# Performance work log

Hardware: AMD Instinct MI355X
Metric: run time of the kernel (lower is better)

## Reference

```python
import jax, jax.numpy as jnp
import numpy as np

EPS = 1e-12  # F.normalize eps


def _l2norm(v, axis=-1):
    # torch.nn.functional.normalize: x / max(||x||_2, eps)
    n = jnp.sqrt(jnp.sum(v * v, axis=axis, keepdims=True))
    return v / jnp.maximum(n, EPS)


def setup_inputs() -> dict:
    key = jax.random.key(0)
    ks = jax.random.split(key, 4)
    B, C, W, H, Z = 8, 256, 16, 16, 16
    N, P = W * H * Z, 64
    heads = 8
    import math
    std_w = 1.0 / math.sqrt(C)      # nn.Linear default-ish scale
    std_ef = 1.0 / math.sqrt(P)     # init_() uses last-dim
    return {
        "x": jax.random.normal(ks[0], (B, C, W, H, Z), dtype=jnp.float32),
        "W_sa": jax.random.uniform(ks[1], (4 * C, C), jnp.float32, -std_w, std_w),
        "EF": jax.random.uniform(ks[2], (N, P), jnp.float32, -std_ef, std_ef),
        "temp2_sa": jnp.ones((heads, 1, 1), jnp.float32),
        "W_sc": jax.random.uniform(ks[3], (4 * C, C), jnp.float32, -std_w, std_w),
        "temp_sc": jnp.ones((heads, 1, 1), jnp.float32),
    }


def _qkvv(xf, Wt, heads):
    # xf: (B, N, C); torch Linear(hidden, 4*hidden, bias=False): y = x @ W.T
    B, N, C = xf.shape
    d = C // heads
    y = xf @ Wt.T                                   # (B, N, 4C)
    y = y.reshape(B, N, 4, heads, d)
    y = jnp.transpose(y, (2, 0, 3, 1, 4))           # (4, B, h, N, d)
    return y[0], y[1], y[2], y[3]


def reference(x, W_sa, EF, temp2_sa, W_sc, temp_sc):
    B, C, W, H, Z = x.shape
    N = W * H * Z
    heads = temp_sc.shape[0]
    d = C // heads
    xf = jnp.transpose(x.reshape(B, C, N), (0, 2, 1))  # (B, N, C)

    # ---- Spatial (Linformer-style projected) attention ----
    q, k, _, v_sa = _qkvv(xf, W_sa, heads)            # each (B, h, N, d)
    q_t = jnp.swapaxes(q, -2, -1)                     # (B, h, d, N)
    k_t = jnp.swapaxes(k, -2, -1)
    v_t = jnp.swapaxes(v_sa, -2, -1)
    k_proj = jnp.einsum('bhdn,nk->bhdk', k_t, EF)     # (B, h, d, P)
    v_proj = jnp.einsum('bhdn,nk->bhdk', v_t, EF)
    q_n = _l2norm(q_t, axis=-1)                       # normalize over N
    attn_sa = jnp.einsum('bhdn,bhdk->bhnk', q_n, k_proj) * temp2_sa  # (B,h,N,P)
    attn_sa = jax.nn.softmax(attn_sa, axis=-1)        # dropout: eval mode (identity)
    x_sa = jnp.einsum('bhnk,bhdk->bhnd', attn_sa, v_proj)            # (B,h,N,d)
    # faithful to original: permute(0,3,1,2) then reshape(B,N,C)
    x_sa = jnp.transpose(x_sa, (0, 3, 1, 2)).reshape(B, N, C)

    # ---- Channel (cross-covariance) attention ----
    qc, kc, v_ca, _ = _qkvv(xf, W_sc, heads)          # (B, h, N, d)
    qc_t = _l2norm(jnp.swapaxes(qc, -2, -1), axis=-1) # (B, h, d, N), norm over N
    kc_t = _l2norm(jnp.swapaxes(kc, -2, -1), axis=-1)
    vc_t = jnp.swapaxes(v_ca, -2, -1)                 # (B, h, d, N)
    attn_ca = jnp.einsum('bhdn,bhen->bhde', qc_t, kc_t) * temp_sc    # (B,h,d,d)
    attn_ca = jax.nn.softmax(attn_ca, axis=-1)
    x_ca = jnp.einsum('bhde,bhen->bhdn', attn_ca, vc_t)              # (B,h,d,N)
    x_ca = jnp.transpose(x_ca, (0, 3, 1, 2)).reshape(B, N, C)        # (B,N,h,d)->(B,N,C)

    feat = x_ca + x_sa
    out = jnp.transpose(feat.reshape(B, W, H, Z, C), (0, 4, 1, 2, 3))
    return out
```

## Files before the change

### kernel.cpp

```cpp
#include <hip/hip_runtime.h>

typedef unsigned short u16;
typedef unsigned int   u32;

typedef __attribute__((ext_vector_type(4))) short short4v;
typedef __attribute__((ext_vector_type(8))) short bf16x8;
typedef __attribute__((ext_vector_type(4))) float f32x4;


__device__ __forceinline__ float bf2f(u16 u){
  union { u32 i; float f; } v; v.i = ((u32)u) << 16; return v.f;
}
__device__ __forceinline__ u16 f2bf(float f){
  u32 u = __float_as_uint(f);
  u32 r = u + 0x7FFFu + ((u >> 16) & 1u);
  return (u16)(r >> 16);
}

__device__ __forceinline__ void gload_lds16(const u16* g, u16* l){
  __builtin_amdgcn_global_load_lds((const __attribute__((address_space(1))) void*)g,
                                   (__attribute__((address_space(3))) void*)l,
                                   16, 0, 0);
}

__global__ void k_detect(const u16* __restrict__ x, u32* __restrict__ flag){
  __shared__ int cnt[256];
  const int t = threadIdx.x;
  int c = 0;
  #pragma unroll
  for(int i = 0; i < 4; i++){
    u16 v = x[t * 4 + i];
    int e = (v >> 7) & 0xFF;
    if(e >= 112 && e <= 134) c++;
  }
  cnt[t] = c;
  __syncthreads();
  for(int s = 128; s > 0; s >>= 1){
    if(t < s) cnt[t] += cnt[t + s];
    __syncthreads();
  }
  if(t == 0) *flag = (cnt[0] < 800) ? 1u : 0u;
}

__global__ __launch_bounds__(256) void k_conv_bf(const void* __restrict__ src,
                                                 u16* __restrict__ dst, int n,
                                                 const u32* __restrict__ flag){
  const int i0 = (blockIdx.x * 256 + threadIdx.x) * 8;
  if(i0 >= n) return;
  const bool isf32 = (*flag != 0);
  if(isf32){
    const float4 a = *(const float4*)((const float*)src + i0);
    const float4 b = *(const float4*)((const float*)src + i0 + 4);
    uint4 o;
    o.x = (u32)f2bf(a.x) | ((u32)f2bf(a.y) << 16);
    o.y = (u32)f2bf(a.z) | ((u32)f2bf(a.w) << 16);
    o.z = (u32)f2bf(b.x) | ((u32)f2bf(b.y) << 16);
    o.w = (u32)f2bf(b.z) | ((u32)f2bf(b.w) << 16);
    *(uint4*)(dst + i0) = o;
  } else {
    *(uint4*)(dst + i0) = *(const uint4*)((const u16*)src + i0);
  }
}

__global__ __launch_bounds__(256) void k_conv_both(const void* __restrict__ src,
                                                   float* __restrict__ dstf,
                                                   u16* __restrict__ dstb, int n,
                                                   int nb,
                                                   const u32* __restrict__ flag){
  const int i0 = (blockIdx.x * 256 + threadIdx.x) * 4;
  if(i0 >= n) return;
  const bool isf32 = (*flag != 0);
  float4 o;
  if(isf32){
    o = *(const float4*)((const float*)src + i0);
  } else {
    const uint2 a = *(const uint2*)((const u16*)src + i0);
    o.x = bf2f((u16)(a.x & 0xFFFF)); o.y = bf2f((u16)(a.x >> 16));
    o.z = bf2f((u16)(a.y & 0xFFFF)); o.w = bf2f((u16)(a.y >> 16));
  }
  *(float4*)(dstf + i0) = o;
  if(i0 < nb){
    uint2 pk;
    pk.x = (u32)f2bf(o.x) | ((u32)f2bf(o.y) << 16);
    pk.y = (u32)f2bf(o.z) | ((u32)f2bf(o.w) << 16);
    *(uint2*)(dstb + i0) = pk;
  }
}

__global__ void k_conv_tf(const void* __restrict__ s0, const void* __restrict__ s1,
                          float* __restrict__ tf, const u32* __restrict__ flag){
  const int t = threadIdx.x;
  if(t >= 16) return;
  const void* s = (t < 8) ? s0 : s1;
  const int i = t & 7;
  if(*flag != 0) tf[t] = ((const float*)s)[i];
  else           tf[t] = bf2f(((const u16*)s)[i]);
}

__global__ __launch_bounds__(256) void k_convT(const void* __restrict__ src,
                                               u16* __restrict__ xb,
                                               u16* __restrict__ xT,
                                               const u32* __restrict__ flag){
  __shared__ u16 T[64][72];
  const int t = threadIdx.x;
  const int n0 = blockIdx.x * 64, c0 = blockIdx.y * 64, b = blockIdx.z;
  const int cl = t >> 2, ns = (t & 3) * 16;
  const bool isf32 = (*flag != 0);
  const size_t srcoff = ((size_t)(b * 256 + c0 + cl)) * 4096 + n0 + ns;
  u16 e[16];
  if(isf32){
    const float* sp = (const float*)src + srcoff;
    #pragma unroll
    for(int i = 0; i < 4; i++){
      const float4 v = *(const float4*)(sp + i * 4);
      e[i*4+0] = f2bf(v.x); e[i*4+1] = f2bf(v.y);
      e[i*4+2] = f2bf(v.z); e[i*4+3] = f2bf(v.w);
    }
  } else {
    const u16* sp = (const u16*)src + srcoff;
    *(uint4*)&e[0] = *(const uint4*)sp;
    *(uint4*)&e[8] = *(const uint4*)(sp + 8);
  }
  u16* xbp = xb + srcoff;
  *(uint4*)xbp       = *(uint4*)&e[0];
  *(uint4*)(xbp + 8) = *(uint4*)&e[8];
  #pragma unroll
  for(int i = 0; i < 16; i++) T[ns + i][cl] = e[i];
  __syncthreads();
  const int nl = t >> 2, cs = (t & 3) * 16;
  u16* xtp = xT + ((size_t)b * 4096 + n0 + nl) * 256 + c0 + cs;
  *(uint4*)xtp       = *(const uint4*)&T[nl][cs];
  *(uint4*)(xtp + 8) = *(const uint4*)&T[nl][cs + 8];
}

__global__ __launch_bounds__(256) void k_conv_efT(const void* __restrict__ src,
                                                  u16* __restrict__ EFT,
                                                  const u32* __restrict__ flag){
  __shared__ u16 T[64][72];
  const int t = threadIdx.x;
  const int n0 = blockIdx.x * 64;
  const int nl = t >> 2, p0 = (t & 3) * 16;
  const bool isf32 = (*flag != 0);
  const size_t off = (size_t)(n0 + nl) * 64 + p0;
  u16 e[16];
  if(isf32){
    const float* sp = (const float*)src + off;
    #pragma unroll
    for(int i = 0; i < 4; i++){
      const float4 v = *(const float4*)(sp + i * 4);
      e[i*4+0] = f2bf(v.x); e[i*4+1] = f2bf(v.y);
      e[i*4+2] = f2bf(v.z); e[i*4+3] = f2bf(v.w);
    }
  } else {
    const u16* sp = (const u16*)src + off;
    *(uint4*)&e[0] = *(const uint4*)sp;
    *(uint4*)&e[8] = *(const uint4*)(sp + 8);
  }
  #pragma unroll
  for(int i = 0; i < 16; i++) T[p0 + i][nl] = e[i];
  __syncthreads();
  const int pr = t >> 2, nn = (t & 3) * 16;
  u16* dp = EFT + (size_t)pr * 4096 + n0 + nn;
  *(uint4*)dp       = *(const uint4*)&T[pr][nn];
  *(uint4*)(dp + 8) = *(const uint4*)&T[pr][nn + 8];
}

__global__ __launch_bounds__(256) void k_qkv(const u16* __restrict__ Wc,
                                             const u16* __restrict__ xT,
                                             u16* __restrict__ Y){
  __shared__ union {
    struct { u16 Ws[128][64]; u16 Xs[128][64]; } s;
    u16 Cs[128][136];
  } L;
  const int t = threadIdx.x;
  const int n0 = blockIdx.x * 128, m0 = blockIdx.y * 128, b = blockIdx.z;
  const int w = t >> 6, lane = t & 63;
  const int fm = lane & 15, fq = lane >> 4;
  const int wm = w >> 1, wn = w & 1;
  const int lr = lane >> 3, lc = (lane & 7) * 8;
  const u16* gw = Wc + (size_t)m0 * 256;
  const u16* gx = xT + ((size_t)b * 4096 + n0) * 256;
  f32x4 acc[4][4] = {};
  for(int kc = 0; kc < 256; kc += 64){
    #pragma unroll
    for(int i = 0; i < 4; i++){
      const int row = w * 32 + i * 8;
      gload_lds16(gw + (size_t)(row + lr) * 256 + kc + lc, &L.s.Ws[row][0]);
      gload_lds16(gx + (size_t)(row + lr) * 256 + kc + lc, &L.s.Xs[row][0]);
    }
    __syncthreads();
    #pragma unroll
    for(int kh = 0; kh < 2; kh++){
      bf16x8 af[4], bx[4];
      #pragma unroll
      for(int mt = 0; mt < 4; mt++)
        af[mt] = *(const bf16x8*)&L.s.Ws[wm * 64 + mt * 16 + fm][kh * 32 + fq * 8];
      #pragma unroll
      for(int nt = 0; nt < 4; nt++)
        bx[nt] = *(const bf16x8*)&L.s.Xs[wn * 64 + nt * 16 + fm][kh * 32 + fq * 8];
      #pragma unroll
      for(int mt = 0; mt < 4; mt++)
        #pragma unroll
        for(int nt = 0; nt < 4; nt++)
          acc[mt][nt] = __builtin_amdgcn_mfma_f32_16x16x32_bf16(af[mt], bx[nt],
                                                                acc[mt][nt], 0, 0, 0);
    }
    __syncthreads();
  }
  #pragma unroll
  for(int mt = 0; mt < 4; mt++)
    #pragma unroll
    for(int nt = 0; nt < 4; nt++)
      #pragma unroll
      for(int r = 0; r < 4; r++)
        L.Cs[wm * 64 + mt * 16 + fq * 4 + r][wn * 64 + nt * 16 + fm] =
          f2bf(acc[mt][nt][r]);
  __syncthreads();
  #pragma unroll
  for(int i = 0; i < 8; i++){
    const int row = i * 16 + (t >> 4), ce = (t & 15) * 8;
    *(uint4*)(Y + ((size_t)b * 1024 + m0 + row) * 4096 + n0 + ce) =
      *(const uint4*)&L.Cs[row][ce];
  }
}

__global__ __launch_bounds__(256) void k_xef_mfma(const u16* __restrict__ xb,
                                                  const u16* __restrict__ EFT,
                                                  float* __restrict__ xefp){
  const int t = threadIdx.x;
  const int mh = blockIdx.x, s = blockIdx.y, b = blockIdx.z;
  const int w = t >> 6, lane = t & 63;
  const int fm = lane & 15, fq = lane >> 4;
  const int c0 = mh * 128 + w * 32;
  const u16* ar = xb + ((size_t)(b * 256 + c0 + fm)) * 4096 + s * 256 + fq * 8;
  const u16* br = EFT + (size_t)fm * 4096 + s * 256 + fq * 8;
  f32x4 acc[2][4] = {};
  #pragma unroll
  for(int kk = 0; kk < 8; kk++){
    bf16x8 bfr[4];
    #pragma unroll
    for(int nt = 0; nt < 4; nt++)
      bfr[nt] = *(const bf16x8*)(br + (size_t)nt * 16 * 4096 + kk * 32);
    #pragma unroll
    for(int mt = 0; mt < 2; mt++){
      bf16x8 af = *(const bf16x8*)(ar + (size_t)mt * 16 * 4096 + kk * 32);
      #pragma unroll
      for(int nt = 0; nt < 4; nt++)
        acc[mt][nt] = __builtin_amdgcn_mfma_f32_16x16x32_bf16(af, bfr[nt],
                                                              acc[mt][nt], 0, 0, 0);
    }
  }
  float* dst = xefp + (size_t)s * 131072 + (size_t)(b * 256 + c0) * 64;
  #pragma unroll
  for(int mt = 0; mt < 2; mt++)
    #pragma unroll
    for(int nt = 0; nt < 4; nt++)
      #pragma unroll
      for(int r = 0; r < 4; r++)
        dst[(mt * 16 + fq * 4 + r) * 64 + nt * 16 + fm] = acc[mt][nt][r];
}

__global__ __launch_bounds__(256) void k_xred(const float* __restrict__ xefp,
                                              float* __restrict__ xef){
  const int i0 = (blockIdx.x * 256 + threadIdx.x) * 4;
  float4 a = *(const float4*)(xefp + i0);
  #pragma unroll
  for(int s = 1; s < 16; s++){
    const float4 v = *(const float4*)(xefp + (size_t)s * 131072 + i0);
    a.x += v.x; a.y += v.y; a.z += v.z; a.w += v.w;
  }
  *(float4*)(xef + i0) = a;
}

__global__ __launch_bounds__(256) void k_kv4b(const float* __restrict__ Wsaf,
                                              const float* __restrict__ xef,
                                              const float* __restrict__ invsa,
                                              u16* __restrict__ kpT,
                                              u16* __restrict__ vpb){
  const int t = threadIdx.x;
  const int ri = t >> 6, p = t & 63;
  const int r = blockIdx.x * 4 + ri, b = blockIdx.y;
  const int row_w = (r < 256) ? (256 + r) : (512 + r);
  const float* wr = Wsaf + (size_t)row_w * 256;
  const float* xr = xef + (size_t)(b * 256) * 64 + p;
  float acc = 0.f;
  for(int c = 0; c < 256; c++)
    acc += wr[c] * xr[(size_t)c * 64];
  if(r < 256){
    const float sc = invsa[b * 256 + r];
    kpT[((size_t)(b * 8 + (r >> 5)) * 64 + p) * 32 + (r & 31)] = f2bf(acc * sc);
  } else {
    const int rv = r - 256;
    vpb[((size_t)(b * 8 + (rv >> 5)) * 32 + (rv & 31)) * 64 + p] = f2bf(acc);
  }
}

__global__ __launch_bounds__(256) void k_norm3(const u16* __restrict__ Y,
                                               float* __restrict__ inv3){
  __shared__ float red[256];
  const int r = blockIdx.x, b = blockIdx.y, t = threadIdx.x;
  const u16* row = Y + (size_t)(b * 1024 + r) * 4096 + t * 16;
  u16 e[16];
  *(uint4*)&e[0] = *(const uint4*)row;
  *(uint4*)&e[8] = *(const uint4*)(row + 8);
  float s = 0.f;
  #pragma unroll
  for(int i = 0; i < 16; i++){ float v = bf2f(e[i]); s += v * v; }
  red[t] = s;
  __syncthreads();
  for(int s2 = 128; s2 > 0; s2 >>= 1){
    if(t < s2) red[t] += red[t + s2];
    __syncthreads();
  }
  if(t == 0)
    inv3[(r >> 8) * 2048 + b * 256 + (r & 255)] =
      1.0f / fmaxf(sqrtf(red[0]), 1e-12f);
}

__device__ __forceinline__ bf16x8 ld_frag8(const u16* p){
  short4v lo = *(const short4v*)p;
  short4v hi = *(const short4v*)(p + 4);
  bf16x8 r;
  r[0]=lo[0]; r[1]=lo[1]; r[2]=lo[2]; r[3]=lo[3];
  r[4]=hi[0]; r[5]=hi[1]; r[6]=hi[2]; r[7]=hi[3];
  return r;
}

__global__ __launch_bounds__(256) void k_gram_mfma(const u16* __restrict__ Y,
                                                   float* __restrict__ Gp){
  const int t = threadIdx.x;
  const int s = blockIdx.x, h = blockIdx.y, b = blockIdx.z;
  const int w = t >> 6, lane = t & 63;
  const int fm = lane & 15, fq = lane >> 4;
  const int j0 = (w >> 1) * 16, e0 = (w & 1) * 16;
  const u16* qrow = Y + (size_t)(b * 1024 + 256 + h * 32 + j0 + fm) * 4096;
  const u16* krow = Y + (size_t)(b * 1024 + 512 + h * 32 + e0 + fm) * 4096;
  f32x4 acc = {};
  const int nb0 = s * 512 + fq * 8;
  #pragma unroll 4
  for(int it = 0; it < 16; it++){
    const int nb = nb0 + it * 32;
    bf16x8 a  = ld_frag8(qrow + nb);
    bf16x8 bb = ld_frag8(krow + nb);
    acc = __builtin_amdgcn_mfma_f32_16x16x32_bf16(a, bb, acc, 0, 0, 0);
  }
  float* dst = Gp + ((size_t)((s * 8 + b) * 8 + h) * 1024);
  #pragma unroll
  for(int r = 0; r < 4; r++)
    dst[(j0 + fq * 4 + r) * 32 + e0 + fm] = acc[r];
}

__global__ void k_softmax_ca(const float* __restrict__ Gp,
                             const float* __restrict__ invq,
                             const float* __restrict__ invk,
                             const float* __restrict__ temp,
                             float* __restrict__ attn){
  const int j = threadIdx.x, h = blockIdx.x, b = blockIdx.y;
  const float tm = temp[h];
  const float iq = invq[b * 256 + h * 32 + j];
  float v[32];
  float m = -1e30f;
  #pragma unroll
  for(int e = 0; e < 32; e++){
    float g = 0.f;
    #pragma unroll
    for(int s = 0; s < 8; s++)
      g += Gp[(size_t)s * 65536 + (size_t)(b * 8 + h) * 1024 + j * 32 + e];
    float val = g * iq * invk[b * 256 + h * 32 + e] * tm;
    v[e] = val; m = fmaxf(m, val);
  }
  float sum = 0.f;
  #pragma unroll
  for(int e = 0; e < 32; e++){ v[e] = __expf(v[e] - m); sum += v[e]; }
  const float inv = 1.0f / sum;
  #pragma unroll
  for(int e = 0; e < 32; e++) attn[(size_t)(b * 8 + h) * 1024 + j * 32 + e] = v[e] * inv;
}

__global__ __launch_bounds__(256) void k_sa_mfma(const u16* __restrict__ Y,
                                                 const u16* __restrict__ kpT,
                                                 const u16* __restrict__ vpb,
                                                 const float* __restrict__ temp2,
                                                 u16* __restrict__ xsa){
  __shared__ u16 As[64][36];
  __shared__ u16 Ks[64][36];
  __shared__ u16 Vs[32][68];
  __shared__ u16 Ps[64][68];
  __shared__ u16 Cs[32][68];
  const int t = threadIdx.x;
  const int ntile = blockIdx.x, h = blockIdx.y, b = blockIdx.z;
  const int n0 = ntile * 64;
  const int w = t >> 6, lane = t & 63;
  const int fm = lane & 15, fq = lane >> 4;
  {
    const int j = t >> 3, ns = (t & 7) * 8;
    const u16* src = Y + (size_t)(b * 1024 + h * 32 + j) * 4096 + n0 + ns;
    uint4 v = *(const uint4*)src;
    u16 e[8]; *(uint4*)e = v;
    #pragma unroll
    for(int i = 0; i < 8; i++) As[ns + i][j] = e[i];
  }
  {
    const int p = t >> 2, jb = (t & 3) * 8;
    *(uint4*)&Ks[p][jb] =
      *(const uint4*)(kpT + ((size_t)(b * 8 + h) * 64 + p) * 32 + jb);
  }
  {
    const int jv = t >> 3, ps = (t & 7) * 8;
    *(uint4*)&Vs[jv][ps] =
      *(const uint4*)(vpb + ((size_t)(b * 8 + h) * 32 + jv) * 64 + ps);
  }
  __syncthreads();
  bf16x8 a = ld_frag8(&As[w * 16 + fm][fq * 8]);
  f32x4 lg[4];
  #pragma unroll
  for(int pt = 0; pt < 4; pt++){
    bf16x8 bk = ld_frag8(&Ks[pt * 16 + fm][fq * 8]);
    f32x4 z = {};
    lg[pt] = __builtin_amdgcn_mfma_f32_16x16x32_bf16(a, bk, z, 0, 0, 0);
  }
  const float tm = temp2[h];
  float sinv[4];
  #pragma unroll
  for(int r = 0; r < 4; r++){
    float v0 = lg[0][r]*tm, v1 = lg[1][r]*tm, v2 = lg[2][r]*tm, v3 = lg[3][r]*tm;
    float mx = fmaxf(fmaxf(v0, v1), fmaxf(v2, v3));
    #pragma unroll
    for(int m = 1; m < 16; m <<= 1) mx = fmaxf(mx, __shfl_xor(mx, m, 16));
    v0 = __expf(v0 - mx); v1 = __expf(v1 - mx);
    v2 = __expf(v2 - mx); v3 = __expf(v3 - mx);
    float s = v0 + v1 + v2 + v3;
    #pragma unroll
    for(int m = 1; m < 16; m <<= 1) s += __shfl_xor(s, m, 16);
    sinv[r] = 1.0f / s;
    const int nrow = w * 16 + fq * 4 + r;
    Ps[nrow][fm]      = f2bf(v0);
    Ps[nrow][16 + fm] = f2bf(v1);
    Ps[nrow][32 + fm] = f2bf(v2);
    Ps[nrow][48 + fm] = f2bf(v3);
  }
  f32x4 o[2] = {};
  #pragma unroll
  for(int ks = 0; ks < 2; ks++){
    bf16x8 ap = ld_frag8(&Ps[w * 16 + fm][ks * 32 + fq * 8]);
    #pragma unroll
    for(int jt = 0; jt < 2; jt++){
      bf16x8 bv = ld_frag8(&Vs[jt * 16 + fm][ks * 32 + fq * 8]);
      o[jt] = __builtin_amdgcn_mfma_f32_16x16x32_bf16(ap, bv, o[jt], 0, 0, 0);
    }
  }
  #pragma unroll
  for(int jt = 0; jt < 2; jt++)
    #pragma unroll
    for(int r = 0; r < 4; r++)
      Cs[jt * 16 + fm][w * 16 + fq * 4 + r] = f2bf(o[jt][r] * sinv[r]);
  __syncthreads();
  {
    const int jv = t >> 3, ns = (t & 7) * 8;
    u16 e[8];
    #pragma unroll
    for(int i = 0; i < 8; i++) e[i] = Cs[jv][ns + i];
    *(uint4*)(xsa + ((size_t)(b * 8 + h) * 32 + jv) * 4096 + n0 + ns) = *(uint4*)e;
  }
}

__global__ __launch_bounds__(256) void k_out_mfma(const u16* __restrict__ Y,
                                                  const float* __restrict__ attn,
                                                  const u16* __restrict__ xsa,
                                                  float* __restrict__ out){
  __shared__ u16 Vt[32][516];
  __shared__ u16 xs[32][16][34];
  __shared__ u16 Ah[32][40];
  __shared__ u16 Al[32][40];
  const int t = threadIdx.x;
  const int jg = blockIdx.x, hc = blockIdx.y, b = blockIdx.z;
  const int nn0 = jg * 512;
  const int w = t >> 6, lane = t & 63;
  const int fm = lane & 15, fq = lane >> 4;
  {
    const float4 v = *(const float4*)(attn + (size_t)(b * 8 + hc) * 1024 + t * 4);
    const int j = t >> 3, e0 = (t & 7) * 4;
    float vv[4] = {v.x, v.y, v.z, v.w};
    #pragma unroll
    for(int i = 0; i < 4; i++){
      u16 hi = f2bf(vv[i]);
      Ah[j][e0 + i] = hi;
      Al[j][e0 + i] = f2bf(vv[i] - bf2f(hi));
    }
  }
  {
    const int e = t >> 3, ch = (t & 7) * 64;
    const u16* src = Y + (size_t)(b * 1024 + 768 + hc * 32 + e) * 4096 + nn0 + ch;
    #pragma unroll
    for(int i = 0; i < 8; i++){
      uint4 v = *(const uint4*)(src + i * 8);
      uint2 lo; lo.x = v.x; lo.y = v.y;
      uint2 hi; hi.x = v.z; hi.y = v.w;
      *(uint2*)&Vt[e][ch + i * 8]     = lo;
      *(uint2*)&Vt[e][ch + i * 8 + 4] = hi;
    }
  }
  #pragma unroll
  for(int rep = 0; rep < 2; rep++){
    const int s = rep * 256 + t;
    const int hj = s >> 4, nh = s & 15;
    const int h = hj & 7, jj = hj >> 3;
    const u16* src = xsa + ((size_t)(b * 8 + h) * 32 + jg * 4 + jj) * 4096 + nh * 256 + hc * 32;
    uint4 v0 = *(const uint4*)src;
    uint4 v1 = *(const uint4*)(src + 8);
    u32* d32 = (u32*)&xs[hj][nh][0];
    d32[0] = v0.x; d32[1] = v0.y; d32[2] = v0.z; d32[3] = v0.w;
    d32[4] = v1.x; d32[5] = v1.y; d32[6] = v1.z; d32[7] = v1.w;
    uint4 v2 = *(const uint4*)(src + 16);
    uint4 v3 = *(const uint4*)(src + 24);
    d32[8]  = v2.x; d32[9]  = v2.y; d32[10] = v2.z; d32[11] = v2.w;
    d32[12] = v3.x; d32[13] = v3.y; d32[14] = v3.z; d32[15] = v3.w;
  }
  __syncthreads();
  bf16x8 ah[2], al[2];
  #pragma unroll
  for(int mt = 0; mt < 2; mt++){
    ah[mt] = *(const bf16x8*)&Ah[mt * 16 + fm][fq * 8];
    al[mt] = *(const bf16x8*)&Al[mt * 16 + fm][fq * 8];
  }
  f32x4 acc[2][8] = {};
  #pragma unroll
  for(int nt = 0; nt < 8; nt++){
    const int colb = w * 128 + nt * 16 + fm;
    bf16x8 bv;
    #pragma unroll
    for(int i = 0; i < 8; i++) bv[i] = (short)Vt[fq * 8 + i][colb];
    #pragma unroll
    for(int mt = 0; mt < 2; mt++){
      acc[mt][nt] = __builtin_amdgcn_mfma_f32_16x16x32_bf16(ah[mt], bv, acc[mt][nt], 0, 0, 0);
      acc[mt][nt] = __builtin_amdgcn_mfma_f32_16x16x32_bf16(al[mt], bv, acc[mt][nt], 0, 0, 0);
    }
  }
  #pragma unroll
  for(int mt = 0; mt < 2; mt++)
    #pragma unroll
    for(int nt = 0; nt < 8; nt++){
      const int col = w * 128 + nt * 16 + fm;
      float* op = out + (size_t)(b * 256 + hc * 32 + mt * 16 + fq * 4) * 4096 + nn0 + col;
      #pragma unroll
      for(int r = 0; r < 4; r++){
        const float sa = bf2f(xs[w * 8 + nt][fm][mt * 16 + fq * 4 + r]);
        op[(size_t)r * 4096] = acc[mt][nt][r] + sa;
      }
    }
}

#define OFF_XB    ((size_t)0)
#define OFF_XT    ((size_t)16777216)
#define OFF_Y     ((size_t)33554432)
#define OFF_WSAF  ((size_t)100663296)
#define OFF_WCAT  ((size_t)101711872)
#define OFF_EFT   ((size_t)102236160)
#define OFF_XEF   ((size_t)103284736)
#define OFF_KPT   ((size_t)103809024)
#define OFF_VPB   ((size_t)104071168)
#define OFF_ISA   ((size_t)104333312)
#define OFF_IQC   ((size_t)104341504)
#define OFF_IKC   ((size_t)104349696)
#define OFF_GP    ((size_t)104357888)
#define OFF_ATT   ((size_t)106455040)
#define OFF_TF    ((size_t)106717184)
#define OFF_FLAG  ((size_t)106717248)
#define OFF_XEFP  OFF_XT

extern "C" void kernel_launch(void* const* d_in, const int* in_sizes, int n_in,
                              void* d_out, int out_size, void* d_ws, size_t ws_size,
                              hipStream_t stream){
  (void)in_sizes; (void)n_in; (void)out_size; (void)ws_size;
  char* ws = (char*)d_ws;
  u16*   xb    = (u16*)  (ws + OFF_XB);
  u16*   xsa   = (u16*)  (ws + OFF_XB);
  u16*   xT    = (u16*)  (ws + OFF_XT);
  u16*   Y     = (u16*)  (ws + OFF_Y);
  float* Wsaf  = (float*)(ws + OFF_WSAF);
  u16*   Wcat  = (u16*)  (ws + OFF_WCAT);
  u16*   EFT   = (u16*)  (ws + OFF_EFT);
  float* xef   = (float*)(ws + OFF_XEF);
  u16*   kpT   = (u16*)  (ws + OFF_KPT);
  u16*   vpb   = (u16*)  (ws + OFF_VPB);
  float* invsa = (float*)(ws + OFF_ISA);
  float* invqc = (float*)(ws + OFF_IQC);
  float* invkc = (float*)(ws + OFF_IKC);
  float* Gp    = (float*)(ws + OFF_GP);
  float* attn  = (float*)(ws + OFF_ATT);
  float* tf    = (float*)(ws + OFF_TF);
  u32*   flag  = (u32*)  (ws + OFF_FLAG);
  float* xefp  = (float*)(ws + OFF_XEFP);
  float* out = (float*)d_out;

  k_detect<<<1, 256, 0, stream>>>((const u16*)d_in[0], flag);
  k_convT<<<dim3(64, 4, 8), 256, 0, stream>>>(d_in[0], xb, xT, flag);
  k_conv_both<<<256, 256, 0, stream>>>(d_in[1], Wsaf, Wcat, 262144, 65536, flag);
  k_conv_efT<<<64, 256, 0, stream>>>(d_in[2], EFT, flag);
  k_conv_bf  <<<96,  256, 0, stream>>>(d_in[4], Wcat + 65536, 196608, flag);
  k_conv_tf  <<<1, 64, 0, stream>>>(d_in[3], d_in[5], tf, flag);

  k_qkv<<<dim3(32, 8, 8), 256, 0, stream>>>(Wcat, xT, Y);
  k_xef_mfma<<<dim3(2, 16, 8), 256, 0, stream>>>(xb, EFT, xefp);
  k_xred<<<128, 256, 0, stream>>>(xefp, xef);
  k_norm3<<<dim3(768, 8), 256, 0, stream>>>(Y, invsa);
  k_kv4b<<<dim3(128, 8), 256, 0, stream>>>(Wsaf, xef, invsa, kpT, vpb);
  k_gram_mfma<<<dim3(8, 8, 8), 256, 0, stream>>>(Y, Gp);
  k_softmax_ca<<<dim3(8, 8), 32, 0, stream>>>(Gp, invqc, invkc, tf + 8, attn);
  k_sa_mfma<<<dim3(64, 8, 8), 256, 0, stream>>>(Y, kpT, vpb, tf, xsa);
  k_out_mfma<<<dim3(8, 8, 8), 256, 0, stream>>>(Y, attn, xsa, out);
}
```

Measured before the change: 217.1 us.

## Fuse row-norm partials into QKV GEMM epilogue and merge small conversion kernels

The QKV GEMM epilogue now computes per-tile partial sums of squares for the first 768 output rows and writes them to a partial buffer. The xef reduction kernel also finalizes the inverse norms. This removes the separate k_norm3 pass that re-read the whole Y tensor. The four weight, EF and temperature conversion kernels are merged into one launch, and the channel softmax runs as 8 blocks of 256 threads instead of 64 blocks of 32. The trade-off is extra shuffle work and partial-buffer traffic in the GEMM epilogue.

```diff
diff --git a/kernel.cpp b/kernel.cpp
--- a/kernel.cpp
+++ b/kernel.cpp
@@ -40,61 +40,6 @@
     __syncthreads();
   }
   if(t == 0) *flag = (cnt[0] < 800) ? 1u : 0u;
-}
-
-__global__ __launch_bounds__(256) void k_conv_bf(const void* __restrict__ src,
-                                                 u16* __restrict__ dst, int n,
-                                                 const u32* __restrict__ flag){
-  const int i0 = (blockIdx.x * 256 + threadIdx.x) * 8;
-  if(i0 >= n) return;
-  const bool isf32 = (*flag != 0);
-  if(isf32){
-    const float4 a = *(const float4*)((const float*)src + i0);
-    const float4 b = *(const float4*)((const float*)src + i0 + 4);
-    uint4 o;
-    o.x = (u32)f2bf(a.x) | ((u32)f2bf(a.y) << 16);
-    o.y = (u32)f2bf(a.z) | ((u32)f2bf(a.w) << 16);
-    o.z = (u32)f2bf(b.x) | ((u32)f2bf(b.y) << 16);
-    o.w = (u32)f2bf(b.z) | ((u32)f2bf(b.w) << 16);
-    *(uint4*)(dst + i0) = o;
-  } else {
-    *(uint4*)(dst + i0) = *(const uint4*)((const u16*)src + i0);
-  }
-}
-
-__global__ __launch_bounds__(256) void k_conv_both(const void* __restrict__ src,
-                                                   float* __restrict__ dstf,
-                                                   u16* __restrict__ dstb, int n,
-                                                   int nb,
-                                                   const u32* __restrict__ flag){
-  const int i0 = (blockIdx.x * 256 + threadIdx.x) * 4;
-  if(i0 >= n) return;
-  const bool isf32 = (*flag != 0);
-  float4 o;
-  if(isf32){
-    o = *(const float4*)((const float*)src + i0);
-  } else {
-    const uint2 a = *(const uint2*)((const u16*)src + i0);
-    o.x = bf2f((u16)(a.x & 0xFFFF)); o.y = bf2f((u16)(a.x >> 16));
-    o.z = bf2f((u16)(a.y & 0xFFFF)); o.w = bf2f((u16)(a.y >> 16));
-  }
-  *(float4*)(dstf + i0) = o;
-  if(i0 < nb){
-    uint2 pk;
-    pk.x = (u32)f2bf(o.x) | ((u32)f2bf(o.y) << 16);
-    pk.y = (u32)f2bf(o.z) | ((u32)f2bf(o.w) << 16);
-    *(uint2*)(dstb + i0) = pk;
-  }
-}
-
-__global__ void k_conv_tf(const void* __restrict__ s0, const void* __restrict__ s1,
-                          float* __restrict__ tf, const u32* __restrict__ flag){
-  const int t = threadIdx.x;
-  if(t >= 16) return;
-  const void* s = (t < 8) ? s0 : s1;
-  const int i = t & 7;
-  if(*flag != 0) tf[t] = ((const float*)s)[i];
-  else           tf[t] = bf2f(((const u16*)s)[i]);
 }
 
 __global__ __launch_bounds__(256) void k_convT(const void* __restrict__ src,
@@ -133,41 +78,90 @@
   *(uint4*)(xtp + 8) = *(const uint4*)&T[nl][cs + 8];
 }
 
-__global__ __launch_bounds__(256) void k_conv_efT(const void* __restrict__ src,
-                                                  u16* __restrict__ EFT,
-                                                  const u32* __restrict__ flag){
+__global__ __launch_bounds__(256) void k_conv_misc(const void* __restrict__ Wsa,
+                                                   const void* __restrict__ EF,
+                                                   const void* __restrict__ Wsc,
+                                                   const void* __restrict__ t2,
+                                                   const void* __restrict__ tsc,
+                                                   float* __restrict__ Wsaf,
+                                                   u16* __restrict__ Wcat,
+                                                   u16* __restrict__ EFT,
+                                                   float* __restrict__ tf,
+                                                   const u32* __restrict__ flag){
   __shared__ u16 T[64][72];
-  const int t = threadIdx.x;
-  const int n0 = blockIdx.x * 64;
-  const int nl = t >> 2, p0 = (t & 3) * 16;
+  const int bx = blockIdx.x, t = threadIdx.x;
   const bool isf32 = (*flag != 0);
-  const size_t off = (size_t)(n0 + nl) * 64 + p0;
-  u16 e[16];
-  if(isf32){
-    const float* sp = (const float*)src + off;
-    #pragma unroll
-    for(int i = 0; i < 4; i++){
-      const float4 v = *(const float4*)(sp + i * 4);
-      e[i*4+0] = f2bf(v.x); e[i*4+1] = f2bf(v.y);
-      e[i*4+2] = f2bf(v.z); e[i*4+3] = f2bf(v.w);
+  if(bx < 256){
+    const int i0 = (bx * 256 + t) * 4;
+    float4 o;
+    if(isf32){
+      o = *(const float4*)((const float*)Wsa + i0);
+    } else {
+      const uint2 a = *(const uint2*)((const u16*)Wsa + i0);
+      o.x = bf2f((u16)(a.x & 0xFFFF)); o.y = bf2f((u16)(a.x >> 16));
+      o.z = bf2f((u16)(a.y & 0xFFFF)); o.w = bf2f((u16)(a.y >> 16));
+    }
+    *(float4*)(Wsaf + i0) = o;
+    if(i0 < 65536){
+      uint2 pk;
+      pk.x = (u32)f2bf(o.x) | ((u32)f2bf(o.y) << 16);
+      pk.y = (u32)f2bf(o.z) | ((u32)f2bf(o.w) << 16);
+      *(uint2*)(Wcat + i0) = pk;
+    }
+  } else if(bx < 320){
+    const int n0 = (bx - 256) * 64;
+    const int nl = t >> 2, p0 = (t & 3) * 16;
+    const size_t off = (size_t)(n0 + nl) * 64 + p0;
+    u16 e[16];
+    if(isf32){
+      const float* sp = (const float*)EF + off;
+      #pragma unroll
+      for(int i = 0; i < 4; i++){
+        const float4 v = *(const float4*)(sp + i * 4);
+        e[i*4+0] = f2bf(v.x); e[i*4+1] = f2bf(v.y);
+        e[i*4+2] = f2bf(v.z); e[i*4+3] = f2bf(v.w);
+      }
+    } else {
+      const u16* sp = (const u16*)EF + off;
+      *(uint4*)&e[0] = *(const uint4*)sp;
+      *(uint4*)&e[8] = *(const uint4*)(sp + 8);
+    }
+    #pragma unroll
+    for(int i = 0; i < 16; i++) T[p0 + i][nl] = e[i];
+    __syncthreads();
+    const int pr = t >> 2, nn = (t & 3) * 16;
+    u16* dp = EFT + (size_t)pr * 4096 + n0 + nn;
+    *(uint4*)dp       = *(const uint4*)&T[pr][nn];
+    *(uint4*)(dp + 8) = *(const uint4*)&T[pr][nn + 8];
+  } else if(bx < 416){
+    const int i0 = ((bx - 320) * 256 + t) * 8;
+    u16* dst = Wcat + 65536;
+    if(isf32){
+      const float4 a = *(const float4*)((const float*)Wsc + i0);
+      const float4 b = *(const float4*)((const float*)Wsc + i0 + 4);
+      uint4 o;
+      o.x = (u32)f2bf(a.x) | ((u32)f2bf(a.y) << 16);
+      o.y = (u32)f2bf(a.z) | ((u32)f2bf(a.w) << 16);
+      o.z = (u32)f2bf(b.x) | ((u32)f2bf(b.y) << 16);
+      o.w = (u32)f2bf(b.z) | ((u32)f2bf(b.w) << 16);
+      *(uint4*)(dst + i0) = o;
+    } else {
+      *(uint4*)(dst + i0) = *(const uint4*)((const u16*)Wsc + i0);
     }
   } else {
-    const u16* sp = (const u16*)src + off;
-    *(uint4*)&e[0] = *(const uint4*)sp;
-    *(uint4*)&e[8] = *(const uint4*)(sp + 8);
-  }
-  #pragma unroll
-  for(int i = 0; i < 16; i++) T[p0 + i][nl] = e[i];
-  __syncthreads();
-  const int pr = t >> 2, nn = (t & 3) * 16;
-  u16* dp = EFT + (size_t)pr * 4096 + n0 + nn;
-  *(uint4*)dp       = *(const uint4*)&T[pr][nn];
-  *(uint4*)(dp + 8) = *(const uint4*)&T[pr][nn + 8];
+    if(t < 16){
+      const void* s = (t < 8) ? t2 : tsc;
+      const int i = t & 7;
+      if(isf32) tf[t] = ((const float*)s)[i];
+      else      tf[t] = bf2f(((const u16*)s)[i]);
+    }
+  }
 }
 
 __global__ __launch_bounds__(256) void k_qkv(const u16* __restrict__ Wc,
                                              const u16* __restrict__ xT,
-                                             u16* __restrict__ Y){
+                                             u16* __restrict__ Y,
+                                             float* __restrict__ nrmp){
   __shared__ union {
     struct { u16 Ws[128][64]; u16 Xs[128][64]; } s;
     u16 Cs[128][136];
@@ -216,11 +210,22 @@
         L.Cs[wm * 64 + mt * 16 + fq * 4 + r][wn * 64 + nt * 16 + fm] =
           f2bf(acc[mt][nt][r]);
   __syncthreads();
+  const bool do_norm = (blockIdx.y < 6);
+  float* npb = nrmp + (size_t)blockIdx.x * 6144 + (size_t)b * 768 + m0;
   #pragma unroll
   for(int i = 0; i < 8; i++){
     const int row = i * 16 + (t >> 4), ce = (t & 15) * 8;
-    *(uint4*)(Y + ((size_t)b * 1024 + m0 + row) * 4096 + n0 + ce) =
-      *(const uint4*)&L.Cs[row][ce];
+    uint4 pk = *(const uint4*)&L.Cs[row][ce];
+    *(uint4*)(Y + ((size_t)b * 1024 + m0 + row) * 4096 + n0 + ce) = pk;
+    if(do_norm){
+      u16 e[8]; *(uint4*)e = pk;
+      float s = 0.f;
+      #pragma unroll
+      for(int k2 = 0; k2 < 8; k2++){ float v = bf2f(e[k2]); s += v * v; }
+      #pragma unroll
+      for(int m2 = 1; m2 < 16; m2 <<= 1) s += __shfl_xor(s, m2, 16);
+      if((t & 15) == 0) npb[row] = s;
+    }
   }
 }
 
@@ -260,16 +265,28 @@
         dst[(mt * 16 + fq * 4 + r) * 64 + nt * 16 + fm] = acc[mt][nt][r];
 }
 
-__global__ __launch_bounds__(256) void k_xred(const float* __restrict__ xefp,
-                                              float* __restrict__ xef){
-  const int i0 = (blockIdx.x * 256 + threadIdx.x) * 4;
-  float4 a = *(const float4*)(xefp + i0);
-  #pragma unroll
-  for(int s = 1; s < 16; s++){
-    const float4 v = *(const float4*)(xefp + (size_t)s * 131072 + i0);
-    a.x += v.x; a.y += v.y; a.z += v.z; a.w += v.w;
-  }
-  *(float4*)(xef + i0) = a;
+__global__ __launch_bounds__(256) void k_xred_nfin(const float* __restrict__ xefp,
+                                                   float* __restrict__ xef,
+                                                   const float* __restrict__ nrmp,
+                                                   float* __restrict__ inv3){
+  const int bx = blockIdx.x, t = threadIdx.x;
+  if(bx < 128){
+    const int i0 = (bx * 256 + t) * 4;
+    float4 a = *(const float4*)(xefp + i0);
+    #pragma unroll
+    for(int s = 1; s < 16; s++){
+      const float4 v = *(const float4*)(xefp + (size_t)s * 131072 + i0);
+      a.x += v.x; a.y += v.y; a.z += v.z; a.w += v.w;
+    }
+    *(float4*)(xef + i0) = a;
+  } else {
+    const int tid = (bx - 128) * 256 + t;
+    float s = 0.f;
+    #pragma unroll
+    for(int nt = 0; nt < 32; nt++) s += nrmp[(size_t)nt * 6144 + tid];
+    const int b = tid / 768, m = tid - b * 768;
+    inv3[(m >> 8) * 2048 + b * 256 + (m & 255)] = 1.0f / fmaxf(sqrtf(s), 1e-12f);
+  }
 }
 
 __global__ __launch_bounds__(256) void k_kv4b(const float* __restrict__ Wsaf,
@@ -295,28 +312,6 @@
   }
 }
 
-__global__ __launch_bounds__(256) void k_norm3(const u16* __restrict__ Y,
-                                               float* __restrict__ inv3){
-  __shared__ float red[256];
-  const int r = blockIdx.x, b = blockIdx.y, t = threadIdx.x;
-  const u16* row = Y + (size_t)(b * 1024 + r) * 4096 + t * 16;
-  u16 e[16];
-  *(uint4*)&e[0] = *(const uint4*)row;
-  *(uint4*)&e[8] = *(const uint4*)(row + 8);
-  float s = 0.f;
-  #pragma unroll
-  for(int i = 0; i < 16; i++){ float v = bf2f(e[i]); s += v * v; }
-  red[t] = s;
-  __syncthreads();
-  for(int s2 = 128; s2 > 0; s2 >>= 1){
-    if(t < s2) red[t] += red[t + s2];
-    __syncthreads();
-  }
-  if(t == 0)
-    inv3[(r >> 8) * 2048 + b * 256 + (r & 255)] =
-      1.0f / fmaxf(sqrtf(red[0]), 1e-12f);
-}
-
 __device__ __forceinline__ bf16x8 ld_frag8(const u16* p){
   short4v lo = *(const short4v*)p;
   short4v hi = *(const short4v*)(p + 4);
@@ -350,12 +345,13 @@
     dst[(j0 + fq * 4 + r) * 32 + e0 + fm] = acc[r];
 }
 
-__global__ void k_softmax_ca(const float* __restrict__ Gp,
+__global__ __launch_bounds__(256) void k_softmax_ca(const float* __restrict__ Gp,
                              const float* __restrict__ invq,
                              const float* __restrict__ invk,
                              const float* __restrict__ temp,
                              float* __restrict__ attn){
-  const int j = threadIdx.x, h = blockIdx.x, b = blockIdx.y;
+  const int t = threadIdx.x, b = blockIdx.x;
+  const int h = t >> 5, j = t & 31;
   const float tm = temp[h];
   const float iq = invq[b * 256 + h * 32 + j];
   float v[32];
@@ -566,6 +562,7 @@
 #define OFF_ATT   ((size_t)106455040)
 #define OFF_TF    ((size_t)106717184)
 #define OFF_FLAG  ((size_t)106717248)
+#define OFF_NRM   ((size_t)106717312)
 #define OFF_XEFP  OFF_XT
 
 extern "C" void kernel_launch(void* const* d_in, const int* in_sizes, int n_in,
@@ -590,23 +587,21 @@
   float* attn  = (float*)(ws + OFF_ATT);
   float* tf    = (float*)(ws + OFF_TF);
   u32*   flag  = (u32*)  (ws + OFF_FLAG);
+  float* nrmp  = (float*)(ws + OFF_NRM);
   float* xefp  = (float*)(ws + OFF_XEFP);
   float* out = (float*)d_out;
 
   k_detect<<<1, 256, 0, stream>>>((const u16*)d_in[0], flag);
   k_convT<<<dim3(64, 4, 8), 256, 0, stream>>>(d_in[0], xb, xT, flag);
-  k_conv_both<<<256, 256, 0, stream>>>(d_in[1], Wsaf, Wcat, 262144, 65536, flag);
-  k_conv_efT<<<64, 256, 0, stream>>>(d_in[2], EFT, flag);
-  k_conv_bf  <<<96,  256, 0, stream>>>(d_in[4], Wcat + 65536, 196608, flag);
-  k_conv_tf  <<<1, 64, 0, stream>>>(d_in[3], d_in[5], tf, flag);
-
-  k_qkv<<<dim3(32, 8, 8), 256, 0, stream>>>(Wcat, xT, Y);
+  k_conv_misc<<<417, 256, 0, stream>>>(d_in[1], d_in[2], d_in[4], d_in[3], d_in[5],
+                                       Wsaf, Wcat, EFT, tf, flag);
+
+  k_qkv<<<dim3(32, 8, 8), 256, 0, stream>>>(Wcat, xT, Y, nrmp);
   k_xef_mfma<<<dim3(2, 16, 8), 256, 0, stream>>>(xb, EFT, xefp);
-  k_xred<<<128, 256, 0, stream>>>(xefp, xef);
-  k_norm3<<<dim3(768, 8), 256, 0, stream>>>(Y, invsa);
+  k_xred_nfin<<<152, 256, 0, stream>>>(xefp, xef, nrmp, invsa);
   k_kv4b<<<dim3(128, 8), 256, 0, stream>>>(Wsaf, xef, invsa, kpT, vpb);
   k_gram_mfma<<<dim3(8, 8, 8), 256, 0, stream>>>(Y, Gp);
-  k_softmax_ca<<<dim3(8, 8), 32, 0, stream>>>(Gp, invqc, invkc, tf + 8, attn);
+  k_softmax_ca<<<8, 256, 0, stream>>>(Gp, invqc, invkc, tf + 8, attn);
   k_sa_mfma<<<dim3(64, 8, 8), 256, 0, stream>>>(Y, kpT, vpb, tf, xsa);
   k_out_mfma<<<dim3(8, 8, 8), 256, 0, stream>>>(Y, attn, xsa, out);
 }
```

New measurement: 211.7 us. 2.5% less time.
